# Performance work log

Hardware: AMD Instinct MI355X
Metric: run time of the kernel (lower is better)

Reference implementation:

```python
import jax, jax.numpy as jnp
import numpy as np

B, L, C = 1, 1536, 768
H, DK, DV, F = 8, 64, 96, 96


def setup_inputs() -> dict:
    key = jax.random.key(0)
    ks = jax.random.split(key, 9)
    s = 0.02
    return {
        "x": jax.random.normal(ks[0], (B, L, C), jnp.float32),
        "Wq": jax.random.normal(ks[1], (C, H * DK), jnp.float32) * s,
        "Wk": jax.random.normal(ks[2], (C, H * DK), jnp.float32) * s,
        "Wv": jax.random.normal(ks[3], (C, H * DV), jnp.float32) * s,
        "Wout": jax.random.normal(ks[4], (H * DV, C), jnp.float32) * s,
        "bout": jnp.zeros((C,), jnp.float32),
        "Wpos": jax.random.normal(ks[5], (F, H * DK), jnp.float32) * s,
        "rel_content_bias": jax.random.normal(ks[6], (1, H, 1, DK), jnp.float32),
        "rel_pos_bias": jax.random.normal(ks[7], (1, H, 1, DK), jnp.float32),
    }


def central_mask_embed(n, features):
    # positions: -(n-1) .. n-1  -> (2n-1,)
    positions = jnp.arange(-(n - 1), n)
    # center widths: 2^1 - 1 .. 2^features - 1
    widths = jnp.float32(2.0) ** jnp.arange(1, features + 1, dtype=jnp.float32) - 1.0
    return (widths[None, :] > jnp.abs(positions).astype(jnp.float32)[:, None]).astype(jnp.float32)


def relative_shift(t):
    # t: (b, h, t1, t2) with t2 = 2*t1 - 1 -> (b, h, t1, t1)
    b, h, t1, t2 = t.shape
    t = jnp.pad(t, ((0, 0), (0, 0), (0, 0), (1, 0)))  # (b,h,t1,t2+1)
    t = t.reshape(b, h, t2 + 1, t1)[:, :, 1:, :]       # (b,h,t2,t1)
    t = t.reshape(b, h, t1, t2)
    return t[..., : (t2 + 2) // 2]


def reference(x, Wq, Wk, Wv, Wout, bout, Wpos, rel_content_bias, rel_pos_bias):
    b, n, _ = x.shape
    q = (x @ Wq).reshape(b, n, H, DK).transpose(0, 2, 1, 3)  # b h n d
    k = (x @ Wk).reshape(b, n, H, DK).transpose(0, 2, 1, 3)
    v = (x @ Wv).reshape(b, n, H, DV).transpose(0, 2, 1, 3)
    q = q / jnp.float32(DK) ** 0.5

    content_logits = jnp.einsum("bhid,bhjd->bhij", q + rel_content_bias, k)

    pos = central_mask_embed(n, F)                 # (2n-1, F)
    pos_k = (pos @ Wpos).reshape(2 * n - 1, H, DK).transpose(1, 0, 2)  # h (2n-1) d
    pos_logits = jnp.einsum("bhid,hjd->bhij", q + rel_pos_bias, pos_k)
    pos_logits = relative_shift(pos_logits)        # (b,h,n,n)

    attn = jax.nn.softmax(content_logits + pos_logits, axis=-1)
    out = jnp.einsum("bhij,bhjd->bhid", attn, v)   # b h n dv
    out = out.transpose(0, 2, 1, 3).reshape(b, n, H * DV)
    return out @ Wout + bout
```

## Files before the change

kernel.cpp:

```cpp
#include <hip/hip_runtime.h>
#include <stdint.h>

#define NTOK 1536
#define CDIM 768
#define NH 8
#define DKH 64
#define DVH 96
#define NF 96

typedef unsigned short u16;
typedef __attribute__((ext_vector_type(8))) short s16x8;
typedef __attribute__((ext_vector_type(4))) float f32x4;

__device__ __forceinline__ float b2f(u16 u) {
    union { uint32_t i; float f; } v; v.i = ((uint32_t)u) << 16; return v.f;
}
__device__ __forceinline__ u16 f2b(float f) {
    union { float f; uint32_t i; } v; v.f = f;
    uint32_t x = v.i;
    return (u16)((x + 0x7FFFu + ((x >> 16) & 1u)) >> 16);
}
__device__ __forceinline__ float ldin(const void* p, int i, int f32) {
    return f32 ? ((const float*)p)[i] : b2f(((const u16*)p)[i]);
}

__device__ __forceinline__ int probe_f32(const void* p) {
    const u16* a = (const u16*)p;
    int lane = threadIdx.x & 63;
    int bad = 0;
#pragma unroll
    for (int t = 0; t < 4; ++t) {
        float v = b2f(a[lane + t * 64]);
        if (!(fabsf(v) < 1e6f)) bad = 1;
    }
    return __ballot(bad) != 0ull;
}

#define FIDX(m, kk) ((((kk) >> 3) * 16 + (m)) * 8 + ((kk) & 7))

#define OFF_WSUF 16
#define OFF_S11  (OFF_WSUF + 5632)
#define OFF_QF   (OFF_S11 + 147456)
#define OFF_KF   (OFF_QF + 393216)
#define OFF_VF   (OFF_KF + 393216)
#define OFF_AOF  (OFF_VF + 589824)
#define OFF_XF   (OFF_AOF + 589824)
#define OFF_WF   (OFF_XF + 589824)
#define OFF_WOF  (OFF_WF + 688128)

__global__ __launch_bounds__(256) void prep(const void* __restrict__ x,
                                            const void* __restrict__ Wq,
                                            const void* __restrict__ Wk,
                                            const void* __restrict__ Wv,
                                            const void* __restrict__ Wout,
                                            const void* __restrict__ Wpos,
                                            float* __restrict__ ws) {
    int bx = blockIdx.x, tid = threadIdx.x;
    int wv = tid >> 6, L = tid & 63;

    if (bx < 11) {
        int t = bx;
        int f = probe_f32(Wpos);
        for (int hd = tid; hd < 512; hd += 256) {
            float s0 = 0.f, s1 = 0.f, s2 = 0.f, s3 = 0.f;
            int f0 = t;
            for (; f0 + 4 <= NF; f0 += 4) {
                s0 += ldin(Wpos, f0 * 512 + hd, f);
                s1 += ldin(Wpos, (f0 + 1) * 512 + hd, f);
                s2 += ldin(Wpos, (f0 + 2) * 512 + hd, f);
                s3 += ldin(Wpos, (f0 + 3) * 512 + hd, f);
            }
            for (; f0 < NF; ++f0) s0 += ldin(Wpos, f0 * 512 + hd, f);
            ws[OFF_WSUF + t * 512 + hd] = (s0 + s1) + (s2 + s3);
        }
        return;
    }
    if (bx < 155) {
        int bxa = bx - 11;
        int f = probe_f32(x);
        u16* dst = (u16*)(ws + OFF_XF);
        int cbase = (bxa * 4 + wv) * 4;
        int m = L & 15, kq = L >> 4;
        int srcs[4];
#pragma unroll
        for (int c = 0; c < 4; ++c) {
            int ch = cbase + c;
            int ti = ch / 24, kc = ch % 24;
            srcs[c] = (ti * 16 + m) * CDIM + kc * 32 + kq * 8;
        }
        if (f) {
            float4 a[4][2];
#pragma unroll
            for (int c = 0; c < 4; ++c) {
                const float* xp = (const float*)x + srcs[c];
                a[c][0] = *(const float4*)(xp);
                a[c][1] = *(const float4*)(xp + 4);
            }
#pragma unroll
            for (int c = 0; c < 4; ++c) {
                union { u16 u[8]; uint4 v; } pk;
                pk.u[0] = f2b(a[c][0].x); pk.u[1] = f2b(a[c][0].y);
                pk.u[2] = f2b(a[c][0].z); pk.u[3] = f2b(a[c][0].w);
                pk.u[4] = f2b(a[c][1].x); pk.u[5] = f2b(a[c][1].y);
                pk.u[6] = f2b(a[c][1].z); pk.u[7] = f2b(a[c][1].w);
                *(uint4*)(dst + (cbase + c) * 512 + L * 8) = pk.v;
            }
        } else {
            uint4 v[4];
#pragma unroll
            for (int c = 0; c < 4; ++c) v[c] = *(const uint4*)((const u16*)x + srcs[c]);
#pragma unroll
            for (int c = 0; c < 4; ++c)
                *(uint4*)(dst + (cbase + c) * 512 + L * 8) = v[c];
        }
        return;
    }
    {
        int c = (bx - 155) * 4 + wv;
        const void* src; int ld, cn0; u16* dst; int kc;
        if (c < 2688) {
            int tn = c / 24; kc = c % 24;
            int n0 = tn * 16;
            dst = (u16*)(ws + OFF_WF) + c * 512;
            if (n0 < 512)       { src = Wq; ld = 512;  cn0 = n0; }
            else if (n0 < 1024) { src = Wk; ld = 512;  cn0 = n0 - 512; }
            else                { src = Wv; ld = CDIM; cn0 = n0 - 1024; }
        } else {
            int c2 = c - 2688;
            int tn = c2 / 24; kc = c2 % 24;
            dst = (u16*)(ws + OFF_WOF) + c2 * 512;
            src = Wout; ld = CDIM; cn0 = tn * 16;
        }
        int f = probe_f32(src);
        int nn = L & 15, kq = L >> 4;
        int base = (kc * 32 + kq * 8) * ld + cn0 + nn;
        union { u16 u[8]; uint4 v; } pk;
        if (f) {
            const float* sp = (const float*)src + base;
            float a0 = sp[0], a1 = sp[ld], a2 = sp[2 * ld], a3 = sp[3 * ld];
            float a4 = sp[4 * ld], a5 = sp[5 * ld], a6 = sp[6 * ld], a7 = sp[7 * ld];
            pk.u[0] = f2b(a0); pk.u[1] = f2b(a1); pk.u[2] = f2b(a2); pk.u[3] = f2b(a3);
            pk.u[4] = f2b(a4); pk.u[5] = f2b(a5); pk.u[6] = f2b(a6); pk.u[7] = f2b(a7);
        } else {
            const u16* sp = (const u16*)src + base;
            pk.u[0] = sp[0]; pk.u[1] = sp[ld]; pk.u[2] = sp[2 * ld]; pk.u[3] = sp[3 * ld];
            pk.u[4] = sp[4 * ld]; pk.u[5] = sp[5 * ld]; pk.u[6] = sp[6 * ld]; pk.u[7] = sp[7 * ld];
        }
        *(uint4*)(dst + L * 8) = pk.v;
    }
}

__global__ __launch_bounds__(256) void qkv_reg(const void* __restrict__ rcb,
                                               const void* __restrict__ rpb,
                                               float* __restrict__ ws) {
    __shared__ float qt[64 * 68];
    __shared__ float rpd[12];
    const u16* xf = (const u16*)(ws + OFF_XF);
    const u16* wf = (const u16*)(ws + OFF_WF);
    u16* qf = (u16*)(ws + OFF_QF);
    u16* kf = (u16*)(ws + OFF_KF);
    u16* vf = (u16*)(ws + OFF_VF);

    int tid = threadIdx.x;
    int lane = tid & 63, w = tid >> 6;
    int quad = lane >> 4, col = lane & 15;
    int ti4 = blockIdx.x;
    int tn4 = blockIdx.y;
    int tn = tn4 * 4 + w;
    int i0 = ti4 * 64;
    bool isQ = (tn4 < 8);
    int hq = tn4;

    s16x8 bw0, bw1;
    int f32p = 0, f32c = 0;
    if (isQ) {
        f32p = probe_f32(rpb);
        f32c = probe_f32(rcb);
        int t = lane & 15, kq = lane >> 4;
        union { u16 u[8]; s16x8 v; } p0, p1;
#pragma unroll
        for (int j = 0; j < 8; ++j) {
            float v0 = 0.f, v1 = 0.f;
            if (t < 11) {
                v0 = ws[OFF_WSUF + t * 512 + hq * 64 + kq * 8 + j];
                v1 = ws[OFF_WSUF + t * 512 + hq * 64 + 32 + kq * 8 + j];
            }
            p0.u[j] = f2b(v0); p1.u[j] = f2b(v1);
        }
        bw0 = p0.v; bw1 = p1.v;
        if (tid < 12) {
            float s0 = 0.f, s1 = 0.f, s2 = 0.f, s3 = 0.f;
            if (tid < 11) {
                const float* wp = ws + OFF_WSUF + tid * 512 + hq * 64;
#pragma unroll 4
                for (int d = 0; d < 64; d += 4) {
                    s0 += ldin(rpb, hq * 64 + d,     f32p) * wp[d];
                    s1 += ldin(rpb, hq * 64 + d + 1, f32p) * wp[d + 1];
                    s2 += ldin(rpb, hq * 64 + d + 2, f32p) * wp[d + 2];
                    s3 += ldin(rpb, hq * 64 + d + 3, f32p) * wp[d + 3];
                }
            }
            rpd[tid] = (s0 + s1) + (s2 + s3);
        }
    }

    f32x4 acc[4];
#pragma unroll
    for (int mt = 0; mt < 4; ++mt) acc[mt] = (f32x4){0.f, 0.f, 0.f, 0.f};

    const u16* bp = wf + (tn * 24) * 512 + lane * 8;
    const u16* ap = xf + (ti4 * 4 * 24) * 512 + lane * 8;
#pragma unroll 4
    for (int kc = 0; kc < 24; ++kc) {
        s16x8 bfrag = *(const s16x8*)(bp + kc * 512);
#pragma unroll
        for (int mt = 0; mt < 4; ++mt) {
            s16x8 afrag = *(const s16x8*)(ap + (mt * 24 + kc) * 512);
            acc[mt] = __builtin_amdgcn_mfma_f32_16x16x32_bf16(afrag, bfrag, acc[mt], 0, 0, 0);
        }
    }

    if (isQ) {
#pragma unroll
        for (int mt = 0; mt < 4; ++mt)
#pragma unroll
            for (int r = 0; r < 4; ++r)
                qt[(mt * 16 + quad * 4 + r) * 68 + w * 16 + col] = acc[mt][r] * 0.125f;
        __syncthreads();
        int m = lane & 15, kq = lane >> 4;
#pragma unroll
        for (int kc2 = 0; kc2 < 2; ++kc2) {
            union { u16 u[8]; uint4 v; } pk;
#pragma unroll
            for (int j = 0; j < 8; ++j) {
                int d = kc2 * 32 + kq * 8 + j;
                pk.u[j] = f2b(qt[(w * 16 + m) * 68 + d] + ldin(rcb, hq * 64 + d, f32c));
            }
            *(uint4*)(qf + (((hq * 96 + ti4 * 4 + w) * 2 + kc2) * 512) + lane * 8) = pk.v;
        }
        union { u16 u[8]; s16x8 v; } qa0, qa1;
#pragma unroll
        for (int j = 0; j < 8; ++j) {
            qa0.u[j] = f2b(qt[(w * 16 + m) * 68 + kq * 8 + j]);
            qa1.u[j] = f2b(qt[(w * 16 + m) * 68 + 32 + kq * 8 + j]);
        }
        f32x4 s11a = (f32x4){0.f, 0.f, 0.f, 0.f};
        s11a = __builtin_amdgcn_mfma_f32_16x16x32_bf16(qa0.v, bw0, s11a, 0, 0, 0);
        s11a = __builtin_amdgcn_mfma_f32_16x16x32_bf16(qa1.v, bw1, s11a, 0, 0, 0);
        if (col < 12) {
            float rp = rpd[col];
            float* s11 = ws + OFF_S11;
#pragma unroll
            for (int r = 0; r < 4; ++r)
                s11[(hq * NTOK + i0 + w * 16 + quad * 4 + r) * 12 + col] = s11a[r] + rp;
        }
    } else if (tn < 64) {
        int h = (tn >> 2) - 8;
        int d = ((tn & 3) * 16) + col;
#pragma unroll
        for (int mt = 0; mt < 4; ++mt) {
            int tj = ti4 * 4 + mt;
#pragma unroll
            for (int r = 0; r < 4; ++r) {
                int nn = quad * 4 + r;
                kf[((h * 96 + tj) * 2 + (d >> 5)) * 512 + FIDX(nn, d & 31)] = f2b(acc[mt][r]);
            }
        }
    } else {
        int c = tn * 16 + col - 1024;
        int h = c / 96, d = c % 96;
        int nt = d >> 4, nn = d & 15;
#pragma unroll
        for (int mt = 0; mt < 4; ++mt) {
#pragma unroll
            for (int r = 0; r < 4; ++r) {
                int j = i0 + mt * 16 + quad * 4 + r;
                int jc = j >> 5, kk = j & 31;
                vf[((h * 48 + jc) * 6 + nt) * 512 + FIDX(nn, kk)] = f2b(acc[mt][r]);
            }
        }
    }
}

__global__ __launch_bounds__(512) void attn_mfma(float* __restrict__ ws) {
    __shared__ float s11b[192];
    __shared__ float lw[8][16];
    __shared__ union {
        alignas(16) u16 pbuf[8][16 * 36];
        float Om[8][16 * 96];
    } sh;

    const u16* qf = (const u16*)(ws + OFF_QF);
    const u16* kf = (const u16*)(ws + OFF_KF);
    const u16* vf = (const u16*)(ws + OFF_VF);
    const float* s11 = ws + OFF_S11;
    u16* aof = (u16*)(ws + OFF_AOF);

    int h = blockIdx.x & 7;
    int ti = blockIdx.x >> 3;
    int i0 = ti * 16;
    int tid = threadIdx.x;
    int wv = tid >> 6, lane = tid & 63;
    int quad = lane >> 4, col = lane & 15;

    if (tid < 192) s11b[tid] = s11[(h * NTOK + i0 + tid / 12) * 12 + tid % 12];
    const u16* qp = qf + ((h * 96 + ti) * 2) * 512 + lane * 8;
    s16x8 a_lo = *(const s16x8*)(qp);
    s16x8 a_hi = *(const s16x8*)(qp + 512);
    __syncthreads();

    f32x4 O[6];
    float lsum[4];
#pragma unroll
    for (int nt = 0; nt < 6; ++nt) O[nt] = (f32x4){0.f, 0.f, 0.f, 0.f};
#pragma unroll
    for (int r = 0; r < 4; ++r) lsum[r] = 0.f;

    const u16* kbase = kf + ((h * 96 + wv * 12) * 2) * 512 + lane * 8;
    s16x8 k0lo = *(const s16x8*)(kbase);
    s16x8 k0hi = *(const s16x8*)(kbase + 512);
    s16x8 k1lo = *(const s16x8*)(kbase + 1024);
    s16x8 k1hi = *(const s16x8*)(kbase + 1536);

    for (int c = 0; c < 6; ++c) {
        f32x4 t0 = (f32x4){0.f, 0.f, 0.f, 0.f};
        f32x4 t1 = (f32x4){0.f, 0.f, 0.f, 0.f};
        t0 = __builtin_amdgcn_mfma_f32_16x16x32_bf16(a_lo, k0lo, t0, 0, 0, 0);
        t0 = __builtin_amdgcn_mfma_f32_16x16x32_bf16(a_hi, k0hi, t0, 0, 0, 0);
        t1 = __builtin_amdgcn_mfma_f32_16x16x32_bf16(a_lo, k1lo, t1, 0, 0, 0);
        t1 = __builtin_amdgcn_mfma_f32_16x16x32_bf16(a_hi, k1hi, t1, 0, 0, 0);
        if (c < 5) {
            const u16* kn = kbase + (c + 1) * 2048;
            k0lo = *(const s16x8*)(kn);
            k0hi = *(const s16x8*)(kn + 512);
            k1lo = *(const s16x8*)(kn + 1024);
            k1hi = *(const s16x8*)(kn + 1536);
        }
        int jc = wv * 6 + c;
        const u16* vp = vf + ((h * 48 + jc) * 6) * 512 + lane * 8;
        s16x8 vr[6];
#pragma unroll
        for (int nt = 0; nt < 6; ++nt) vr[nt] = *(const s16x8*)(vp + nt * 512);
        int j0 = wv * 192 + c * 32;
        int lo1 = j0 - (i0 + 15), lo2 = i0 - (j0 + 31);
        int dmin = lo1 > 0 ? lo1 : (lo2 > 0 ? lo2 : 0);
        int dm1 = i0 + 15 - j0, dm2 = j0 + 31 - i0;
        int dmax = dm1 > dm2 ? dm1 : dm2;
        int tlo = 31 - __builtin_clz(dmin + 1);
        int thi = 31 - __builtin_clz(dmax + 1);
        if (tlo == thi) {
#pragma unroll
            for (int r = 0; r < 4; ++r) {
                int row = quad * 4 + r;
                float bv = s11b[row * 12 + tlo] - 12.f;
                float p0 = __expf(t0[r] + bv);
                float p1 = __expf(t1[r] + bv);
                sh.pbuf[wv][row * 36 + col] = f2b(p0);
                sh.pbuf[wv][row * 36 + 16 + col] = f2b(p1);
                lsum[r] += p0 + p1;
            }
        } else {
#pragma unroll
            for (int r = 0; r < 4; ++r) {
                int row = quad * 4 + r;
                int ig = i0 + row;
                int d0 = ig - (j0 + col); d0 = d0 < 0 ? -d0 : d0;
                int d1 = ig - (j0 + 16 + col); d1 = d1 < 0 ? -d1 : d1;
                float v0 = t0[r] + s11b[row * 12 + (31 - __builtin_clz(d0 + 1))];
                float v1 = t1[r] + s11b[row * 12 + (31 - __builtin_clz(d1 + 1))];
                float p0 = __expf(v0 - 12.f);
                float p1 = __expf(v1 - 12.f);
                sh.pbuf[wv][row * 36 + col] = f2b(p0);
                sh.pbuf[wv][row * 36 + 16 + col] = f2b(p1);
                lsum[r] += p0 + p1;
            }
        }
        const u16* pr = &sh.pbuf[wv][col * 36 + quad * 8];
        union { s16x8 v; uint2 u2[2]; } pa;
        pa.u2[0] = *(const uint2*)(pr);
        pa.u2[1] = *(const uint2*)(pr + 4);
#pragma unroll
        for (int nt = 0; nt < 6; ++nt)
            O[nt] = __builtin_amdgcn_mfma_f32_16x16x32_bf16(pa.v, vr[nt], O[nt], 0, 0, 0);
    }

#pragma unroll
    for (int off = 1; off < 16; off <<= 1)
#pragma unroll
        for (int r = 0; r < 4; ++r) lsum[r] += __shfl_xor(lsum[r], off);
    if (col == 0)
#pragma unroll
        for (int r = 0; r < 4; ++r) lw[wv][quad * 4 + r] = lsum[r];
    __syncthreads();
#pragma unroll
    for (int r = 0; r < 4; ++r) {
        int row = quad * 4 + r;
#pragma unroll
        for (int nt = 0; nt < 6; ++nt)
            sh.Om[wv][row * 96 + nt * 16 + col] = O[nt][r];
    }
    __syncthreads();
    for (int idx = tid; idx < 16 * 96; idx += 512) {
        int row = idx / 96, cc = idx % 96;
        float L = 0.f, val = 0.f;
#pragma unroll
        for (int v = 0; v < 8; ++v) { L += lw[v][row]; val += sh.Om[v][idx]; }
        aof[(ti * 24 + h * 3 + (cc >> 5)) * 512 + FIDX(row, cc & 31)] = f2b(val / L);
    }
}

__global__ __launch_bounds__(256) void out_reg(const void* __restrict__ bout,
                                               float* __restrict__ ws,
                                               float* __restrict__ out) {
    const u16* af = (const u16*)(ws + OFF_AOF);
    const u16* wof = (const u16*)(ws + OFF_WOF);
    int f32b = probe_f32(bout);

    int tid = threadIdx.x;
    int lane = tid & 63, w = tid >> 6;
    int quad = lane >> 4, col = lane & 15;
    int ti4 = blockIdx.x;
    int tn = blockIdx.y * 4 + w;
    int i0 = ti4 * 64;
    int n0 = blockIdx.y * 64;

    f32x4 acc[4];
#pragma unroll
    for (int mt = 0; mt < 4; ++mt) acc[mt] = (f32x4){0.f, 0.f, 0.f, 0.f};

    const u16* bp = wof + (tn * 24) * 512 + lane * 8;
    const u16* ap = af + (ti4 * 4 * 24) * 512 + lane * 8;
#pragma unroll 4
    for (int kc = 0; kc < 24; ++kc) {
        s16x8 bfrag = *(const s16x8*)(bp + kc * 512);
#pragma unroll
        for (int mt = 0; mt < 4; ++mt) {
            s16x8 afrag = *(const s16x8*)(ap + (mt * 24 + kc) * 512);
            acc[mt] = __builtin_amdgcn_mfma_f32_16x16x32_bf16(afrag, bfrag, acc[mt], 0, 0, 0);
        }
    }

    int c = n0 + w * 16 + col;
    float bias = ldin(bout, c, f32b);
#pragma unroll
    for (int mt = 0; mt < 4; ++mt) {
#pragma unroll
        for (int r = 0; r < 4; ++r) {
            int i = i0 + mt * 16 + quad * 4 + r;
            out[i * CDIM + c] = acc[mt][r] + bias;
        }
    }
}

extern "C" void kernel_launch(void* const* d_in, const int* in_sizes, int n_in,
                              void* d_out, int out_size, void* d_ws, size_t ws_size,
                              hipStream_t stream) {
    float* out = (float*)d_out;
    float* ws = (float*)d_ws;

    const int want[9] = {1179648, 393216, 393216, 589824, 589824, 768, 49152, 512, 512};
    int role2in[9], used[9] = {0};
    bool ok = (n_in == 9);
    if (ok) {
        for (int r = 0; r < 9; ++r) {
            int found = -1;
            for (int i = 0; i < 9 && found < 0; ++i)
                if (!used[i] && in_sizes[i] == want[r]) found = i;
            if (found < 0) { ok = false; break; }
            used[found] = 1;
            role2in[r] = found;
        }
    }
    if (!ok) for (int r = 0; r < 9; ++r) role2in[r] = r;

    const void* x    = d_in[role2in[0]];
    const void* Wq   = d_in[role2in[1]];
    const void* Wk   = d_in[role2in[2]];
    const void* Wv   = d_in[role2in[3]];
    const void* Wout = d_in[role2in[4]];
    const void* bout = d_in[role2in[5]];
    const void* Wpos = d_in[role2in[6]];
    const void* rcb  = d_in[role2in[7]];
    const void* rpb  = d_in[role2in[8]];

    hipLaunchKernelGGL(prep, dim3(1115), dim3(256), 0, stream,
                       x, Wq, Wk, Wv, Wout, Wpos, ws);
    hipLaunchKernelGGL(qkv_reg, dim3(24, 28), dim3(256), 0, stream,
                       rcb, rpb, ws);
    hipLaunchKernelGGL(attn_mfma, dim3(768), dim3(512), 0, stream, ws);
    hipLaunchKernelGGL(out_reg, dim3(24, 12), dim3(256), 0, stream,
                       bout, ws, out);
}
```

Before: 143.0 us.

## Process two 16-row query tiles per attention block to reuse K and V fragments

Each attention block now handles 32 query rows (two 16-row tiles) instead of 16, halving the grid to 384 blocks. Each loaded K and V fragment feeds MFMAs for both tiles, halving global K/V traffic per query row. The cost is more registers per thread (two accumulator sets, two score tiles), a second shared P buffer, and a serialized two-pass epilogue. Fewer blocks may reduce occupancy and wave-level parallelism on a 256-CU device.

```diff
diff --git a/kernel.cpp b/kernel.cpp
--- a/kernel.cpp
+++ b/kernel.cpp
@@ -282,11 +282,14 @@
     }
 }
 
-__global__ __launch_bounds__(512) void attn_mfma(float* __restrict__ ws) {
-    __shared__ float s11b[192];
+__global__ __launch_bounds__(512, 4) void attn_mfma(float* __restrict__ ws) {
+    __shared__ float s11b[384];
     __shared__ float lw[8][16];
     __shared__ union {
-        alignas(16) u16 pbuf[8][16 * 36];
+        struct {
+            alignas(16) u16 pbufA[8][16 * 36];
+            alignas(16) u16 pbufB[8][16 * 36];
+        };
         float Om[8][16 * 96];
     } sh;
 
@@ -297,24 +300,29 @@
     u16* aof = (u16*)(ws + OFF_AOF);
 
     int h = blockIdx.x & 7;
-    int ti = blockIdx.x >> 3;
-    int i0 = ti * 16;
+    int ti2 = blockIdx.x >> 3;
+    int i0 = ti2 * 32;
     int tid = threadIdx.x;
     int wv = tid >> 6, lane = tid & 63;
     int quad = lane >> 4, col = lane & 15;
 
-    if (tid < 192) s11b[tid] = s11[(h * NTOK + i0 + tid / 12) * 12 + tid % 12];
-    const u16* qp = qf + ((h * 96 + ti) * 2) * 512 + lane * 8;
-    s16x8 a_lo = *(const s16x8*)(qp);
-    s16x8 a_hi = *(const s16x8*)(qp + 512);
+    if (tid < 384) s11b[tid] = s11[(h * NTOK + i0 + tid / 12) * 12 + tid % 12];
+    const u16* qp0 = qf + ((h * 96 + ti2 * 2) * 2) * 512 + lane * 8;
+    s16x8 a0lo = *(const s16x8*)(qp0);
+    s16x8 a0hi = *(const s16x8*)(qp0 + 512);
+    s16x8 a1lo = *(const s16x8*)(qp0 + 1024);
+    s16x8 a1hi = *(const s16x8*)(qp0 + 1536);
     __syncthreads();
 
-    f32x4 O[6];
-    float lsum[4];
-#pragma unroll
-    for (int nt = 0; nt < 6; ++nt) O[nt] = (f32x4){0.f, 0.f, 0.f, 0.f};
-#pragma unroll
-    for (int r = 0; r < 4; ++r) lsum[r] = 0.f;
+    f32x4 O0[6], O1[6];
+    float lsum0[4], lsum1[4];
+#pragma unroll
+    for (int nt = 0; nt < 6; ++nt) {
+        O0[nt] = (f32x4){0.f, 0.f, 0.f, 0.f};
+        O1[nt] = (f32x4){0.f, 0.f, 0.f, 0.f};
+    }
+#pragma unroll
+    for (int r = 0; r < 4; ++r) { lsum0[r] = 0.f; lsum1[r] = 0.f; }
 
     const u16* kbase = kf + ((h * 96 + wv * 12) * 2) * 512 + lane * 8;
     s16x8 k0lo = *(const s16x8*)(kbase);
@@ -325,10 +333,16 @@
     for (int c = 0; c < 6; ++c) {
         f32x4 t0 = (f32x4){0.f, 0.f, 0.f, 0.f};
         f32x4 t1 = (f32x4){0.f, 0.f, 0.f, 0.f};
-        t0 = __builtin_amdgcn_mfma_f32_16x16x32_bf16(a_lo, k0lo, t0, 0, 0, 0);
-        t0 = __builtin_amdgcn_mfma_f32_16x16x32_bf16(a_hi, k0hi, t0, 0, 0, 0);
-        t1 = __builtin_amdgcn_mfma_f32_16x16x32_bf16(a_lo, k1lo, t1, 0, 0, 0);
-        t1 = __builtin_amdgcn_mfma_f32_16x16x32_bf16(a_hi, k1hi, t1, 0, 0, 0);
+        f32x4 u0 = (f32x4){0.f, 0.f, 0.f, 0.f};
+        f32x4 u1 = (f32x4){0.f, 0.f, 0.f, 0.f};
+        t0 = __builtin_amdgcn_mfma_f32_16x16x32_bf16(a0lo, k0lo, t0, 0, 0, 0);
+        t0 = __builtin_amdgcn_mfma_f32_16x16x32_bf16(a0hi, k0hi, t0, 0, 0, 0);
+        t1 = __builtin_amdgcn_mfma_f32_16x16x32_bf16(a0lo, k1lo, t1, 0, 0, 0);
+        t1 = __builtin_amdgcn_mfma_f32_16x16x32_bf16(a0hi, k1hi, t1, 0, 0, 0);
+        u0 = __builtin_amdgcn_mfma_f32_16x16x32_bf16(a1lo, k0lo, u0, 0, 0, 0);
+        u0 = __builtin_amdgcn_mfma_f32_16x16x32_bf16(a1hi, k0hi, u0, 0, 0, 0);
+        u1 = __builtin_amdgcn_mfma_f32_16x16x32_bf16(a1lo, k1lo, u1, 0, 0, 0);
+        u1 = __builtin_amdgcn_mfma_f32_16x16x32_bf16(a1hi, k1hi, u1, 0, 0, 0);
         if (c < 5) {
             const u16* kn = kbase + (c + 1) * 2048;
             k0lo = *(const s16x8*)(kn);
@@ -336,68 +350,110 @@
             k1lo = *(const s16x8*)(kn + 1024);
             k1hi = *(const s16x8*)(kn + 1536);
         }
+        int j0 = wv * 192 + c * 32;
+        {
+            int i0g = i0;
+            int lo1 = j0 - (i0g + 15), lo2 = i0g - (j0 + 31);
+            int dmin = lo1 > 0 ? lo1 : (lo2 > 0 ? lo2 : 0);
+            int dm1 = i0g + 15 - j0, dm2 = j0 + 31 - i0g;
+            int dmax = dm1 > dm2 ? dm1 : dm2;
+            int tlo = 31 - __builtin_clz(dmin + 1);
+            int thi = 31 - __builtin_clz(dmax + 1);
+            if (tlo == thi) {
+#pragma unroll
+                for (int r = 0; r < 4; ++r) {
+                    int row = quad * 4 + r;
+                    float bv = s11b[row * 12 + tlo] - 12.f;
+                    float p0 = __expf(t0[r] + bv);
+                    float p1 = __expf(t1[r] + bv);
+                    sh.pbufA[wv][row * 36 + col] = f2b(p0);
+                    sh.pbufA[wv][row * 36 + 16 + col] = f2b(p1);
+                    lsum0[r] += p0 + p1;
+                }
+            } else {
+#pragma unroll
+                for (int r = 0; r < 4; ++r) {
+                    int row = quad * 4 + r;
+                    int ig = i0g + row;
+                    int d0 = ig - (j0 + col); d0 = d0 < 0 ? -d0 : d0;
+                    int d1 = ig - (j0 + 16 + col); d1 = d1 < 0 ? -d1 : d1;
+                    float v0 = t0[r] + s11b[row * 12 + (31 - __builtin_clz(d0 + 1))];
+                    float v1 = t1[r] + s11b[row * 12 + (31 - __builtin_clz(d1 + 1))];
+                    float p0 = __expf(v0 - 12.f);
+                    float p1 = __expf(v1 - 12.f);
+                    sh.pbufA[wv][row * 36 + col] = f2b(p0);
+                    sh.pbufA[wv][row * 36 + 16 + col] = f2b(p1);
+                    lsum0[r] += p0 + p1;
+                }
+            }
+        }
+        {
+            int i0g = i0 + 16;
+            int lo1 = j0 - (i0g + 15), lo2 = i0g - (j0 + 31);
+            int dmin = lo1 > 0 ? lo1 : (lo2 > 0 ? lo2 : 0);
+            int dm1 = i0g + 15 - j0, dm2 = j0 + 31 - i0g;
+            int dmax = dm1 > dm2 ? dm1 : dm2;
+            int tlo = 31 - __builtin_clz(dmin + 1);
+            int thi = 31 - __builtin_clz(dmax + 1);
+            if (tlo == thi) {
+#pragma unroll
+                for (int r = 0; r < 4; ++r) {
+                    int row = quad * 4 + r;
+                    float bv = s11b[(16 + row) * 12 + tlo] - 12.f;
+                    float p0 = __expf(u0[r] + bv);
+                    float p1 = __expf(u1[r] + bv);
+                    sh.pbufB[wv][row * 36 + col] = f2b(p0);
+                    sh.pbufB[wv][row * 36 + 16 + col] = f2b(p1);
+                    lsum1[r] += p0 + p1;
+                }
+            } else {
+#pragma unroll
+                for (int r = 0; r < 4; ++r) {
+                    int row = quad * 4 + r;
+                    int ig = i0g + row;
+                    int d0 = ig - (j0 + col); d0 = d0 < 0 ? -d0 : d0;
+                    int d1 = ig - (j0 + 16 + col); d1 = d1 < 0 ? -d1 : d1;
+                    float v0 = u0[r] + s11b[(16 + row) * 12 + (31 - __builtin_clz(d0 + 1))];
+                    float v1 = u1[r] + s11b[(16 + row) * 12 + (31 - __builtin_clz(d1 + 1))];
+                    float p0 = __expf(v0 - 12.f);
+                    float p1 = __expf(v1 - 12.f);
+                    sh.pbufB[wv][row * 36 + col] = f2b(p0);
+                    sh.pbufB[wv][row * 36 + 16 + col] = f2b(p1);
+                    lsum1[r] += p0 + p1;
+                }
+            }
+        }
         int jc = wv * 6 + c;
+        const u16* prA = &sh.pbufA[wv][col * 36 + quad * 8];
+        const u16* prB = &sh.pbufB[wv][col * 36 + quad * 8];
+        union { s16x8 v; uint2 u2[2]; } pa, pb;
+        pa.u2[0] = *(const uint2*)(prA);
+        pa.u2[1] = *(const uint2*)(prA + 4);
+        pb.u2[0] = *(const uint2*)(prB);
+        pb.u2[1] = *(const uint2*)(prB + 4);
         const u16* vp = vf + ((h * 48 + jc) * 6) * 512 + lane * 8;
-        s16x8 vr[6];
-#pragma unroll
-        for (int nt = 0; nt < 6; ++nt) vr[nt] = *(const s16x8*)(vp + nt * 512);
-        int j0 = wv * 192 + c * 32;
-        int lo1 = j0 - (i0 + 15), lo2 = i0 - (j0 + 31);
-        int dmin = lo1 > 0 ? lo1 : (lo2 > 0 ? lo2 : 0);
-        int dm1 = i0 + 15 - j0, dm2 = j0 + 31 - i0;
-        int dmax = dm1 > dm2 ? dm1 : dm2;
-        int tlo = 31 - __builtin_clz(dmin + 1);
-        int thi = 31 - __builtin_clz(dmax + 1);
-        if (tlo == thi) {
-#pragma unroll
-            for (int r = 0; r < 4; ++r) {
-                int row = quad * 4 + r;
-                float bv = s11b[row * 12 + tlo] - 12.f;
-                float p0 = __expf(t0[r] + bv);
-                float p1 = __expf(t1[r] + bv);
-                sh.pbuf[wv][row * 36 + col] = f2b(p0);
-                sh.pbuf[wv][row * 36 + 16 + col] = f2b(p1);
-                lsum[r] += p0 + p1;
-            }
-        } else {
-#pragma unroll
-            for (int r = 0; r < 4; ++r) {
-                int row = quad * 4 + r;
-                int ig = i0 + row;
-                int d0 = ig - (j0 + col); d0 = d0 < 0 ? -d0 : d0;
-                int d1 = ig - (j0 + 16 + col); d1 = d1 < 0 ? -d1 : d1;
-                float v0 = t0[r] + s11b[row * 12 + (31 - __builtin_clz(d0 + 1))];
-                float v1 = t1[r] + s11b[row * 12 + (31 - __builtin_clz(d1 + 1))];
-                float p0 = __expf(v0 - 12.f);
-                float p1 = __expf(v1 - 12.f);
-                sh.pbuf[wv][row * 36 + col] = f2b(p0);
-                sh.pbuf[wv][row * 36 + 16 + col] = f2b(p1);
-                lsum[r] += p0 + p1;
-            }
-        }
-        const u16* pr = &sh.pbuf[wv][col * 36 + quad * 8];
-        union { s16x8 v; uint2 u2[2]; } pa;
-        pa.u2[0] = *(const uint2*)(pr);
-        pa.u2[1] = *(const uint2*)(pr + 4);
-#pragma unroll
-        for (int nt = 0; nt < 6; ++nt)
-            O[nt] = __builtin_amdgcn_mfma_f32_16x16x32_bf16(pa.v, vr[nt], O[nt], 0, 0, 0);
+#pragma unroll
+        for (int nt = 0; nt < 6; ++nt) {
+            s16x8 vfr = *(const s16x8*)(vp + nt * 512);
+            O0[nt] = __builtin_amdgcn_mfma_f32_16x16x32_bf16(pa.v, vfr, O0[nt], 0, 0, 0);
+            O1[nt] = __builtin_amdgcn_mfma_f32_16x16x32_bf16(pb.v, vfr, O1[nt], 0, 0, 0);
+        }
     }
 
 #pragma unroll
     for (int off = 1; off < 16; off <<= 1)
 #pragma unroll
-        for (int r = 0; r < 4; ++r) lsum[r] += __shfl_xor(lsum[r], off);
+        for (int r = 0; r < 4; ++r) lsum0[r] += __shfl_xor(lsum0[r], off);
     if (col == 0)
 #pragma unroll
-        for (int r = 0; r < 4; ++r) lw[wv][quad * 4 + r] = lsum[r];
+        for (int r = 0; r < 4; ++r) lw[wv][quad * 4 + r] = lsum0[r];
     __syncthreads();
 #pragma unroll
     for (int r = 0; r < 4; ++r) {
         int row = quad * 4 + r;
 #pragma unroll
         for (int nt = 0; nt < 6; ++nt)
-            sh.Om[wv][row * 96 + nt * 16 + col] = O[nt][r];
+            sh.Om[wv][row * 96 + nt * 16 + col] = O0[nt][r];
     }
     __syncthreads();
     for (int idx = tid; idx < 16 * 96; idx += 512) {
@@ -405,7 +461,32 @@
         float L = 0.f, val = 0.f;
 #pragma unroll
         for (int v = 0; v < 8; ++v) { L += lw[v][row]; val += sh.Om[v][idx]; }
-        aof[(ti * 24 + h * 3 + (cc >> 5)) * 512 + FIDX(row, cc & 31)] = f2b(val / L);
+        aof[((ti2 * 2) * 24 + h * 3 + (cc >> 5)) * 512 + FIDX(row, cc & 31)] = f2b(val / L);
+    }
+    __syncthreads();
+
+#pragma unroll
+    for (int off = 1; off < 16; off <<= 1)
+#pragma unroll
+        for (int r = 0; r < 4; ++r) lsum1[r] += __shfl_xor(lsum1[r], off);
+    if (col == 0)
+#pragma unroll
+        for (int r = 0; r < 4; ++r) lw[wv][quad * 4 + r] = lsum1[r];
+    __syncthreads();
+#pragma unroll
+    for (int r = 0; r < 4; ++r) {
+        int row = quad * 4 + r;
+#pragma unroll
+        for (int nt = 0; nt < 6; ++nt)
+            sh.Om[wv][row * 96 + nt * 16 + col] = O1[nt][r];
+    }
+    __syncthreads();
+    for (int idx = tid; idx < 16 * 96; idx += 512) {
+        int row = idx / 96, cc = idx % 96;
+        float L = 0.f, val = 0.f;
+#pragma unroll
+        for (int v = 0; v < 8; ++v) { L += lw[v][row]; val += sh.Om[v][idx]; }
+        aof[((ti2 * 2 + 1) * 24 + h * 3 + (cc >> 5)) * 512 + FIDX(row, cc & 31)] = f2b(val / L);
     }
 }
 
@@ -487,7 +568,7 @@
                        x, Wq, Wk, Wv, Wout, Wpos, ws);
     hipLaunchKernelGGL(qkv_reg, dim3(24, 28), dim3(256), 0, stream,
                        rcb, rpb, ws);
-    hipLaunchKernelGGL(attn_mfma, dim3(768), dim3(512), 0, stream, ws);
+    hipLaunchKernelGGL(attn_mfma, dim3(384), dim3(512), 0, stream, ws);
     hipLaunchKernelGGL(out_reg, dim3(24, 12), dim3(256), 0, stream,
                        bout, ws, out);
 }
```

Result: slower. 166.8 us (+16.6%).
